# Kernel optimization log

Measured on AMD Instinct MI355X. Metric: run time of the kernel, lower is better.

Reference implementation:

```python
import jax, jax.numpy as jnp
import numpy as np

B, N, D = 8, 2048, 128

def setup_inputs() -> dict:
    key = jax.random.key(0)
    k1, k2, k3 = jax.random.split(key, 3)
    embeddings = jax.random.normal(k1, (B, N, D), dtype=jnp.float32)
    cost_matrix = jax.random.uniform(k2, (B, N, N), dtype=jnp.float32)
    W = jax.random.normal(k3, (D, 2 * D), dtype=jnp.float32) * (1.0 / np.sqrt(2 * D))
    b = jnp.zeros((D,), dtype=jnp.float32)
    return {"embeddings": embeddings, "cost_matrix": cost_matrix, "W": W, "b": b}

def reference(embeddings, cost_matrix, W, b):
    # degree[b,j] = number of nonzero entries in row j of cost_matrix
    degree = (cost_matrix != 0).astype(embeddings.dtype).sum(axis=-1)  # [B,N]
    # sum_neighbors[b,j,d] = sum_i embeddings[b,i,d] * cost_matrix[b,i,j]
    # (algebraic rewrite of the O(B*N*N*D) broadcast-multiply-reduce)
    sum_neighbors = jnp.einsum('bij,bid->bjd', cost_matrix, embeddings)
    sum_neighbors = sum_neighbors / degree[..., None]
    concatenated = jnp.concatenate([embeddings, sum_neighbors], axis=-1)  # [B,N,2D]
    return jax.nn.relu(jnp.einsum('bnf,df->bnd', concatenated, W) + b)
```

## Files before the change

kernel.cpp:

```cpp
#include <hip/hip_runtime.h>
#include <stdint.h>

#define B_ 8
#define N_ 2048
#define D_ 128
#define NT_ 32
#define KT_ 8
#define TILE_BYTES 16384
#define PS_ ((size_t)B_ * N_ * D_)

typedef unsigned short u16;
typedef unsigned int u32;
using f32x4 = __attribute__((ext_vector_type(4))) float;
using bf16x8 = __attribute__((ext_vector_type(8))) short;
using u16x8 = __attribute__((ext_vector_type(8))) u16;

__device__ inline u16 f2bf(float x) {
  u32 u = __float_as_uint(x);
  return (u16)((u + 0x7FFFu + ((u >> 16) & 1u)) >> 16);
}
__device__ inline float bf2f(u16 h) { return __uint_as_float((u32)h << 16); }

__device__ inline void glds16(const void* g, void* l) {
  __builtin_amdgcn_global_load_lds((const __attribute__((address_space(1))) void*)g,
                                   (__attribute__((address_space(3))) void*)l, 16, 0, 0);
}

__global__ __launch_bounds__(256) void prep_kernel(const float* __restrict__ E,
                                                   const float* __restrict__ W,
                                                   u16* __restrict__ ETsw,
                                                   u16* __restrict__ Wfrag) {
  const int blk = blockIdx.x;
  const int t = threadIdx.x;
  if (blk == 256) {
#pragma unroll
    for (int i = 0; i < 16; ++i) {
      const int idx = i * 256 + t;
      const int lane = idx & 63;
      const int kf = (idx >> 6) & 7;
      const int fn = (idx >> 9) & 1;
      const int wv = idx >> 10;
      const int d = wv * 32 + fn * 16 + (lane & 15);
      const int kb = kf * 32 + (lane >> 4) * 8;
      u16x8 pk;
#pragma unroll
      for (int e = 0; e < 8; ++e) pk[e] = f2bf(W[d * 256 + kb + e]);
      *(u16x8*)(Wfrag + (size_t)idx * 8) = pk;
    }
    return;
  }
  __shared__ float Els[64][132];
  const int b = blk >> 5;
  const int g = blk & 31;
  const float* Eb = E + ((size_t)b * N_ + g * 64) * D_;
#pragma unroll
  for (int s = 0; s < 8; ++s) {
    const int f4 = t + 256 * s;
    const int r = f4 >> 5;
    const int c4 = f4 & 31;
    f32x4 v = *(const f32x4*)(Eb + (size_t)r * D_ + c4 * 4);
#pragma unroll
    for (int e = 0; e < 4; ++e) Els[r][c4 * 4 + e] = v[e];
  }
  __syncthreads();
  u16* img = ETsw + ((size_t)b * NT_ + g) * (TILE_BYTES / 2);
  const int d = t >> 1;
  const int swz = (d ^ (d >> 3)) & 7;
#pragma unroll
  for (int gg = 0; gg < 4; ++gg) {
    const int grp = (t & 1) * 4 + gg;
    u16x8 pk;
#pragma unroll
    for (int e = 0; e < 8; ++e) pk[e] = f2bf(Els[grp * 8 + e][d]);
    *(u16x8*)(img + d * 64 + ((grp ^ swz) << 3)) = pk;
  }
}

__global__ __launch_bounds__(256) void gemm_kernel(const float* __restrict__ C,
                                                   const u16* __restrict__ ETsw,
                                                   u16* __restrict__ Sp,
                                                   int* __restrict__ zeros) {
  __shared__ __align__(16) u16 Asw[2][64 * 64];
  __shared__ __align__(16) u16 Bsw[2][128 * 64];
  const int phys = blockIdx.x;
  const int orig = (phys & 7) * 128 + (phys >> 3);
  const int b = orig >> 7;
  const int ks = (orig >> 5) & 3;
  const int jt = orig & 31;
  const int j0 = jt * 64;
  const int t = threadIdx.x;
  const int lane = t & 63;
  const int wave = t >> 6;
  const int wm = wave >> 1, wn = wave & 1;
  const int lm = lane & 15, lh = lane >> 4;
  const int aRow = t >> 4, aCol = t & 15;

  const float* Cb = C + (size_t)b * N_ * N_;
  const char* Eimg = (const char*)(ETsw + (size_t)b * NT_ * (TILE_BYTES / 2));
  int* zb = zeros + b * N_;
  const int g0 = ks * KT_;

  f32x4 acc[2][4];
#pragma unroll
  for (int i = 0; i < 2; ++i)
#pragma unroll
    for (int j = 0; j < 4; ++j) acc[i][j] = (f32x4)0.0f;
  f32x4 av[2][4];

#define ISSUE_B(gi, buf)                                                          \
  {                                                                               \
    _Pragma("unroll") for (int s = 0; s < 4; ++s) {                               \
      const int chunk = s * 4 + wave;                                             \
      glds16(Eimg + (size_t)(gi)*TILE_BYTES + chunk * 1024 + lane * 16,           \
             (char*)&Bsw[buf][0] + chunk * 1024);                                 \
    }                                                                             \
  }
#define LOAD_A(gi, slot)                                                          \
  {                                                                               \
    _Pragma("unroll") for (int s = 0; s < 4; ++s) av[slot][s] =                   \
        *(const f32x4*)(Cb + (size_t)((gi)*64 + aRow + 16 * s) * N_ + j0 + aCol * 4); \
  }
#define WRITE_A(gi, buf, slot)                                                    \
  {                                                                               \
    _Pragma("unroll") for (int s = 0; s < 4; ++s) {                               \
      const int i = aRow + 16 * s;                                                \
      f32x4 v = av[slot][s];                                                      \
      int zc = (v[0] == 0.0f) + (v[1] == 0.0f) + (v[2] == 0.0f) + (v[3] == 0.0f);\
      if (__any(zc)) {                         \
        if (zc) atomicAdd(&zb[(gi)*64 + i], zc);                                  \
      }                                                                           \
      _Pragma("unroll") for (int e = 0; e < 4; ++e) {                             \
        const int jl = aCol * 4 + e;                                              \
        const int sz = (jl ^ (jl >> 3)) & 7;                                      \
        Asw[buf][jl * 64 + (i ^ (sz << 3))] = f2bf(v[e]);                         \
      }                                                                           \
    }                                                                             \
  }
#define MFMA_PHASE(buf)                                                           \
  {                                                                               \
    bf16x8 af[2][2], bfr[4][2];                                                   \
    _Pragma("unroll") for (int fm = 0; fm < 2; ++fm) {                            \
      const int jl = wm * 32 + fm * 16 + lm;                                      \
      const int sz = (jl ^ (jl >> 3)) & 7;                                        \
      _Pragma("unroll") for (int kf = 0; kf < 2; ++kf) {                          \
        const int K8 = kf * 32 + lh * 8;                                          \
        af[fm][kf] = *(const bf16x8*)&Asw[buf][jl * 64 + (K8 ^ (sz << 3))];       \
      }                                                                           \
    }                                                                             \
    _Pragma("unroll") for (int fn = 0; fn < 4; ++fn) {                            \
      const int nl = wn * 64 + fn * 16 + lm;                                      \
      const int sz = (nl ^ (nl >> 3)) & 7;                                        \
      _Pragma("unroll") for (int kf = 0; kf < 2; ++kf) {                          \
        const int K8 = kf * 32 + lh * 8;                                          \
        bfr[fn][kf] = *(const bf16x8*)&Bsw[buf][nl * 64 + (K8 ^ (sz << 3))];      \
      }                                                                           \
    }                                                                             \
    _Pragma("unroll") for (int kf = 0; kf < 2; ++kf)                              \
        _Pragma("unroll") for (int fm = 0; fm < 2; ++fm)                          \
        _Pragma("unroll") for (int fn = 0; fn < 4; ++fn) acc[fm][fn] =            \
        __builtin_amdgcn_mfma_f32_16x16x32_bf16(af[fm][kf], bfr[fn][kf],          \
                                                acc[fm][fn], 0, 0, 0);            \
  }
#define STEP(kt, DOLOAD, VMSTR)                                                   \
  ISSUE_B(g0 + (kt) + 1, ((kt) + 1) & 1);                                         \
  __builtin_amdgcn_sched_barrier(0);                                              \
  MFMA_PHASE((kt) & 1);                                                           \
  __builtin_amdgcn_sched_barrier(0);                                              \
  WRITE_A(g0 + (kt) + 1, ((kt) + 1) & 1, (kt) & 1);                               \
  __builtin_amdgcn_sched_barrier(0);                                              \
  if (DOLOAD) LOAD_A(g0 + (kt) + 3, (kt) & 1);                                    \
  __builtin_amdgcn_sched_barrier(0);                                              \
  asm volatile("s_waitcnt " VMSTR ::: "memory");                                  \
  asm volatile("s_waitcnt lgkmcnt(0)" ::: "memory");                              \
  __builtin_amdgcn_sched_barrier(0);                                              \
  __builtin_amdgcn_s_barrier();                                                   \
  __builtin_amdgcn_sched_barrier(0);

  ISSUE_B(g0, 0);
  LOAD_A(g0, 0);
  WRITE_A(g0, 0, 0);
  LOAD_A(g0 + 1, 0);
  LOAD_A(g0 + 2, 1);
  asm volatile("s_waitcnt lgkmcnt(0)" ::: "memory");
  __builtin_amdgcn_sched_barrier(0);
  __builtin_amdgcn_s_barrier();
  __builtin_amdgcn_sched_barrier(0);

  STEP(0, 1, "vmcnt(4)")
  STEP(1, 1, "vmcnt(4)")
  STEP(2, 1, "vmcnt(4)")
  STEP(3, 1, "vmcnt(4)")
  STEP(4, 1, "vmcnt(4)")
  STEP(5, 0, "vmcnt(0)")
  STEP(6, 0, "vmcnt(0)")
  MFMA_PHASE(1)

  u16* Sb = Sp + (size_t)ks * PS_ + ((size_t)b * N_ + j0) * D_;
#pragma unroll
  for (int fm = 0; fm < 2; ++fm)
#pragma unroll
    for (int fn = 0; fn < 4; ++fn)
#pragma unroll
      for (int r = 0; r < 4; ++r) {
        const int row = wm * 32 + fm * 16 + lh * 4 + r;
        const int col = wn * 64 + fn * 16 + lm;
        Sb[(size_t)row * D_ + col] = f2bf(acc[fm][fn][r]);
      }
#undef ISSUE_B
#undef LOAD_A
#undef WRITE_A
#undef MFMA_PHASE
#undef STEP
}

__global__ __launch_bounds__(256) void out_kernel(const float* __restrict__ E,
                                                  const u16* __restrict__ Sp,
                                                  const int* __restrict__ zeros,
                                                  const u16* __restrict__ Wfrag,
                                                  const float* __restrict__ bias,
                                                  float* __restrict__ out) {
  __shared__ __align__(16) u16 Als[32 * 256];
  const int r0 = blockIdx.x * 32;
  const int t = threadIdx.x;
  const int lane = t & 63;
  const int wave = t >> 6;
  const int lm = lane & 15, lh = lane >> 4;

  bf16x8 wf[2][8];
#pragma unroll
  for (int fn = 0; fn < 2; ++fn)
#pragma unroll
    for (int kf = 0; kf < 8; ++kf)
      wf[fn][kf] = *(const bf16x8*)(Wfrag +
          (((size_t)(wave * 2 + fn) * 8 + kf) * 64 + lane) * 8);

  const int r = t >> 3, gq = t & 7;
  const int swzr = (r ^ (r >> 3)) & 7;
  const float idg = 1.0f / (2048.0f - (float)zeros[r0 + r]);
  const float* Er = E + (size_t)(r0 + r) * D_;
#pragma unroll
  for (int h = 0; h < 2; ++h) {
    const int k8 = gq + 8 * h;
    f32x4 v0 = *(const f32x4*)(Er + k8 * 8);
    f32x4 v1 = *(const f32x4*)(Er + k8 * 8 + 4);
    u16x8 pk;
#pragma unroll
    for (int e = 0; e < 4; ++e) { pk[e] = f2bf(v0[e]); pk[4 + e] = f2bf(v1[e]); }
    *(u16x8*)&Als[r * 256 + ((k8 ^ swzr) << 3)] = pk;
  }
  const size_t off = (size_t)(r0 + r) * D_;
#pragma unroll
  for (int h = 0; h < 2; ++h) {
    const int kq = gq + 8 * h;
    u16x8 p0 = *(const u16x8*)(Sp + 0 * PS_ + off + kq * 8);
    u16x8 p1 = *(const u16x8*)(Sp + 1 * PS_ + off + kq * 8);
    u16x8 p2 = *(const u16x8*)(Sp + 2 * PS_ + off + kq * 8);
    u16x8 p3 = *(const u16x8*)(Sp + 3 * PS_ + off + kq * 8);
    u16x8 pk;
#pragma unroll
    for (int e = 0; e < 8; ++e) {
      float sum = (bf2f(p0[e]) + bf2f(p1[e])) + (bf2f(p2[e]) + bf2f(p3[e]));
      pk[e] = f2bf(sum * idg);
    }
    *(u16x8*)&Als[r * 256 + (((16 + kq) ^ swzr) << 3)] = pk;
  }
  __syncthreads();

  f32x4 acc[2][2];
#pragma unroll
  for (int i = 0; i < 2; ++i)
#pragma unroll
    for (int j = 0; j < 2; ++j) acc[i][j] = (f32x4)0.0f;
  const int dbase = wave * 32;
#pragma unroll
  for (int kf = 0; kf < 8; ++kf) {
    bf16x8 af[2];
#pragma unroll
    for (int fm = 0; fm < 2; ++fm) {
      const int rr = fm * 16 + lm;
      const int sz = (rr ^ (rr >> 3)) & 7;
      af[fm] = *(const bf16x8*)&Als[rr * 256 + (((kf * 4 + lh) ^ sz) << 3)];
    }
#pragma unroll
    for (int fm = 0; fm < 2; ++fm)
#pragma unroll
      for (int fn = 0; fn < 2; ++fn)
        acc[fm][fn] = __builtin_amdgcn_mfma_f32_16x16x32_bf16(af[fm], wf[fn][kf],
                                                              acc[fm][fn], 0, 0, 0);
  }
  float bb[2] = {bias[dbase + lm], bias[dbase + 16 + lm]};
#pragma unroll
  for (int fm = 0; fm < 2; ++fm)
#pragma unroll
    for (int fn = 0; fn < 2; ++fn)
#pragma unroll
      for (int rr = 0; rr < 4; ++rr) {
        const int row = r0 + fm * 16 + lh * 4 + rr;
        const int d = dbase + fn * 16 + lm;
        float x = acc[fm][fn][rr] + bb[fn];
        out[(size_t)row * D_ + d] = x > 0.0f ? x : 0.0f;
      }
}

extern "C" void kernel_launch(void* const* d_in, const int* in_sizes, int n_in,
                              void* d_out, int out_size, void* d_ws, size_t ws_size,
                              hipStream_t stream) {
  (void)in_sizes; (void)n_in; (void)out_size; (void)ws_size;
  const float* E = (const float*)d_in[0];
  const float* C = (const float*)d_in[1];
  const float* W = (const float*)d_in[2];
  const float* bias = (const float*)d_in[3];
  float* out = (float*)d_out;

  char* ws = (char*)d_ws;
  int* zeros = (int*)ws;
  u16* ETsw = (u16*)(ws + 65536);
  u16* Wfrag = (u16*)(ws + 65536 + 4194304);
  u16* Sp = (u16*)(ws + 65536 + 4194304 + 65536);

  hipMemsetAsync(zeros, 0, B_ * N_ * sizeof(int), stream);
  hipLaunchKernelGGL(prep_kernel, dim3(257), dim3(256), 0, stream, E, W, ETsw, Wfrag);
  hipLaunchKernelGGL(gemm_kernel, dim3(1024), dim3(256), 0, stream, C, ETsw, Sp, zeros);
  hipLaunchKernelGGL(out_kernel, dim3(512), dim3(256), 0, stream, E, Sp, zeros, Wfrag, bias, out);
}
```

Before: 223.3 us.

## Reassociate neighbor aggregation to multiply embeddings by W first

The prep kernel now computes E·W1 and G = E·W2 with MFMA. The big cost-matrix GEMM then multiplies C^T by G instead of by E, so the final kernel becomes an elementwise combine: EW1 + H·inv_degree + bias, then ReLU. This removes the second dense GEMM from the output stage. In exchange it adds an fp32 EW1 buffer and rounds G to bf16 before the large GEMM, which changes the rounding error. The dominant C GEMM stays the same size.

```diff
diff --git a/kernel.cpp b/kernel.cpp
--- a/kernel.cpp
+++ b/kernel.cpp
@@ -26,59 +26,107 @@
                                    (__attribute__((address_space(3))) void*)l, 16, 0, 0);
 }
 
-__global__ __launch_bounds__(256) void prep_kernel(const float* __restrict__ E,
-                                                   const float* __restrict__ W,
-                                                   u16* __restrict__ ETsw,
-                                                   u16* __restrict__ Wfrag) {
+__global__ __launch_bounds__(256) void prep2_kernel(const float* __restrict__ E,
+                                                    const float* __restrict__ W,
+                                                    u16* __restrict__ Gimg,
+                                                    float* __restrict__ EW1) {
+  __shared__ __align__(16) u16 SH[64 * 128];
   const int blk = blockIdx.x;
+  const int b = blk >> 5;
+  const int it = blk & 31;
+  const int i0 = it * 64;
   const int t = threadIdx.x;
-  if (blk == 256) {
-#pragma unroll
-    for (int i = 0; i < 16; ++i) {
-      const int idx = i * 256 + t;
-      const int lane = idx & 63;
-      const int kf = (idx >> 6) & 7;
-      const int fn = (idx >> 9) & 1;
-      const int wv = idx >> 10;
-      const int d = wv * 32 + fn * 16 + (lane & 15);
-      const int kb = kf * 32 + (lane >> 4) * 8;
-      u16x8 pk;
-#pragma unroll
-      for (int e = 0; e < 8; ++e) pk[e] = f2bf(W[d * 256 + kb + e]);
-      *(u16x8*)(Wfrag + (size_t)idx * 8) = pk;
+  const int lane = t & 63;
+  const int wave = t >> 6;
+  const int lm = lane & 15, lh = lane >> 4;
+
+  const float* Eb = E + ((size_t)b * N_ + i0) * D_;
+#pragma unroll
+  for (int c = 0; c < 4; ++c) {
+    const int chunk = c * 256 + t;
+    const int i = chunk >> 4;
+    const int k8 = chunk & 15;
+    f32x4 v0 = *(const f32x4*)(Eb + i * D_ + k8 * 8);
+    f32x4 v1 = *(const f32x4*)(Eb + i * D_ + k8 * 8 + 4);
+    u16x8 pk;
+#pragma unroll
+    for (int e = 0; e < 4; ++e) { pk[e] = f2bf(v0[e]); pk[4 + e] = f2bf(v1[e]); }
+    *(u16x8*)&SH[i * 128 + ((k8 ^ (i & 7)) << 3)] = pk;
+  }
+  __syncthreads();
+
+  const int dbase = wave * 32;
+  f32x4 acc1[4][2], accG[4][2];
+#pragma unroll
+  for (int fm = 0; fm < 4; ++fm)
+#pragma unroll
+    for (int fn = 0; fn < 2; ++fn) { acc1[fm][fn] = (f32x4)0.0f; accG[fm][fn] = (f32x4)0.0f; }
+#pragma unroll
+  for (int kf = 0; kf < 4; ++kf) {
+    bf16x8 af[4];
+#pragma unroll
+    for (int fm = 0; fm < 4; ++fm) {
+      const int i = fm * 16 + lm;
+      af[fm] = *(const bf16x8*)&SH[i * 128 + (((kf * 4 + lh) ^ (i & 7)) << 3)];
     }
-    return;
-  }
-  __shared__ float Els[64][132];
-  const int b = blk >> 5;
-  const int g = blk & 31;
-  const float* Eb = E + ((size_t)b * N_ + g * 64) * D_;
-#pragma unroll
-  for (int s = 0; s < 8; ++s) {
-    const int f4 = t + 256 * s;
-    const int r = f4 >> 5;
-    const int c4 = f4 & 31;
-    f32x4 v = *(const f32x4*)(Eb + (size_t)r * D_ + c4 * 4);
-#pragma unroll
-    for (int e = 0; e < 4; ++e) Els[r][c4 * 4 + e] = v[e];
-  }
+#pragma unroll
+    for (int fn = 0; fn < 2; ++fn) {
+      const int d = dbase + fn * 16 + lm;
+      const float* wr = W + d * 256 + kf * 32 + lh * 8;
+      f32x4 a0 = *(const f32x4*)(wr);
+      f32x4 a1 = *(const f32x4*)(wr + 4);
+      f32x4 b0 = *(const f32x4*)(wr + 128);
+      f32x4 b1 = *(const f32x4*)(wr + 132);
+      u16x8 w1, w2;
+#pragma unroll
+      for (int e = 0; e < 4; ++e) {
+        w1[e] = f2bf(a0[e]); w1[4 + e] = f2bf(a1[e]);
+        w2[e] = f2bf(b0[e]); w2[4 + e] = f2bf(b1[e]);
+      }
+      bf16x8 w1f = *(bf16x8*)&w1;
+      bf16x8 w2f = *(bf16x8*)&w2;
+#pragma unroll
+      for (int fm = 0; fm < 4; ++fm) {
+        acc1[fm][fn] = __builtin_amdgcn_mfma_f32_16x16x32_bf16(af[fm], w1f, acc1[fm][fn], 0, 0, 0);
+        accG[fm][fn] = __builtin_amdgcn_mfma_f32_16x16x32_bf16(af[fm], w2f, accG[fm][fn], 0, 0, 0);
+      }
+    }
+  }
+  float* EWb = EW1 + ((size_t)b * N_ + i0) * D_;
+#pragma unroll
+  for (int fm = 0; fm < 4; ++fm)
+#pragma unroll
+    for (int fn = 0; fn < 2; ++fn)
+#pragma unroll
+      for (int rr = 0; rr < 4; ++rr)
+        EWb[(fm * 16 + lh * 4 + rr) * D_ + dbase + fn * 16 + lm] = acc1[fm][fn][rr];
+
   __syncthreads();
-  u16* img = ETsw + ((size_t)b * NT_ + g) * (TILE_BYTES / 2);
+#pragma unroll
+  for (int fm = 0; fm < 4; ++fm)
+#pragma unroll
+    for (int fn = 0; fn < 2; ++fn)
+#pragma unroll
+      for (int rr = 0; rr < 4; ++rr) {
+        const int d = dbase + fn * 16 + lm;
+        const int il = fm * 16 + lh * 4 + rr;
+        SH[d * 64 + ((((il >> 3) ^ (d & 7)) << 3) | (il & 7))] = f2bf(accG[fm][fn][rr]);
+      }
+  __syncthreads();
+  u16* img = Gimg + ((size_t)b * NT_ + it) * (TILE_BYTES / 2);
   const int d = t >> 1;
   const int swz = (d ^ (d >> 3)) & 7;
 #pragma unroll
   for (int gg = 0; gg < 4; ++gg) {
     const int grp = (t & 1) * 4 + gg;
-    u16x8 pk;
-#pragma unroll
-    for (int e = 0; e < 8; ++e) pk[e] = f2bf(Els[grp * 8 + e][d]);
+    u16x8 pk = *(const u16x8*)&SH[d * 64 + ((grp ^ (d & 7)) << 3)];
     *(u16x8*)(img + d * 64 + ((grp ^ swz) << 3)) = pk;
   }
 }
 
 __global__ __launch_bounds__(256) void gemm_kernel(const float* __restrict__ C,
-                                                   const u16* __restrict__ ETsw,
-                                                   u16* __restrict__ Sp,
+                                                   const u16* __restrict__ Gimg,
+                                                   u16* __restrict__ Hp,
                                                    int* __restrict__ zeros) {
   __shared__ __align__(16) u16 Asw[2][64 * 64];
   __shared__ __align__(16) u16 Bsw[2][128 * 64];
@@ -96,7 +144,7 @@
   const int aRow = t >> 4, aCol = t & 15;
 
   const float* Cb = C + (size_t)b * N_ * N_;
-  const char* Eimg = (const char*)(ETsw + (size_t)b * NT_ * (TILE_BYTES / 2));
+  const char* Bimg = (const char*)(Gimg + (size_t)b * NT_ * (TILE_BYTES / 2));
   int* zb = zeros + b * N_;
   const int g0 = ks * KT_;
 
@@ -111,7 +159,7 @@
   {                                                                               \
     _Pragma("unroll") for (int s = 0; s < 4; ++s) {                               \
       const int chunk = s * 4 + wave;                                             \
-      glds16(Eimg + (size_t)(gi)*TILE_BYTES + chunk * 1024 + lane * 16,           \
+      glds16(Bimg + (size_t)(gi)*TILE_BYTES + chunk * 1024 + lane * 16,           \
              (char*)&Bsw[buf][0] + chunk * 1024);                                 \
     }                                                                             \
   }
@@ -195,7 +243,7 @@
   STEP(6, 0, "vmcnt(0)")
   MFMA_PHASE(1)
 
-  u16* Sb = Sp + (size_t)ks * PS_ + ((size_t)b * N_ + j0) * D_;
+  u16* Hb = Hp + (size_t)ks * PS_ + ((size_t)b * N_ + j0) * D_;
 #pragma unroll
   for (int fm = 0; fm < 2; ++fm)
 #pragma unroll
@@ -204,7 +252,7 @@
       for (int r = 0; r < 4; ++r) {
         const int row = wm * 32 + fm * 16 + lh * 4 + r;
         const int col = wn * 64 + fn * 16 + lm;
-        Sb[(size_t)row * D_ + col] = f2bf(acc[fm][fn][r]);
+        Hb[(size_t)row * D_ + col] = f2bf(acc[fm][fn][r]);
       }
 #undef ISSUE_B
 #undef LOAD_A
@@ -213,93 +261,36 @@
 #undef STEP
 }
 
-__global__ __launch_bounds__(256) void out_kernel(const float* __restrict__ E,
-                                                  const u16* __restrict__ Sp,
-                                                  const int* __restrict__ zeros,
-                                                  const u16* __restrict__ Wfrag,
-                                                  const float* __restrict__ bias,
-                                                  float* __restrict__ out) {
-  __shared__ __align__(16) u16 Als[32 * 256];
-  const int r0 = blockIdx.x * 32;
-  const int t = threadIdx.x;
-  const int lane = t & 63;
-  const int wave = t >> 6;
-  const int lm = lane & 15, lh = lane >> 4;
-
-  bf16x8 wf[2][8];
-#pragma unroll
-  for (int fn = 0; fn < 2; ++fn)
-#pragma unroll
-    for (int kf = 0; kf < 8; ++kf)
-      wf[fn][kf] = *(const bf16x8*)(Wfrag +
-          (((size_t)(wave * 2 + fn) * 8 + kf) * 64 + lane) * 8);
-
-  const int r = t >> 3, gq = t & 7;
-  const int swzr = (r ^ (r >> 3)) & 7;
-  const float idg = 1.0f / (2048.0f - (float)zeros[r0 + r]);
-  const float* Er = E + (size_t)(r0 + r) * D_;
-#pragma unroll
-  for (int h = 0; h < 2; ++h) {
-    const int k8 = gq + 8 * h;
-    f32x4 v0 = *(const f32x4*)(Er + k8 * 8);
-    f32x4 v1 = *(const f32x4*)(Er + k8 * 8 + 4);
-    u16x8 pk;
-#pragma unroll
-    for (int e = 0; e < 4; ++e) { pk[e] = f2bf(v0[e]); pk[4 + e] = f2bf(v1[e]); }
-    *(u16x8*)&Als[r * 256 + ((k8 ^ swzr) << 3)] = pk;
-  }
-  const size_t off = (size_t)(r0 + r) * D_;
-#pragma unroll
-  for (int h = 0; h < 2; ++h) {
-    const int kq = gq + 8 * h;
-    u16x8 p0 = *(const u16x8*)(Sp + 0 * PS_ + off + kq * 8);
-    u16x8 p1 = *(const u16x8*)(Sp + 1 * PS_ + off + kq * 8);
-    u16x8 p2 = *(const u16x8*)(Sp + 2 * PS_ + off + kq * 8);
-    u16x8 p3 = *(const u16x8*)(Sp + 3 * PS_ + off + kq * 8);
-    u16x8 pk;
-#pragma unroll
-    for (int e = 0; e < 8; ++e) {
-      float sum = (bf2f(p0[e]) + bf2f(p1[e])) + (bf2f(p2[e]) + bf2f(p3[e]));
-      pk[e] = f2bf(sum * idg);
-    }
-    *(u16x8*)&Als[r * 256 + (((16 + kq) ^ swzr) << 3)] = pk;
-  }
-  __syncthreads();
-
-  f32x4 acc[2][2];
-#pragma unroll
-  for (int i = 0; i < 2; ++i)
-#pragma unroll
-    for (int j = 0; j < 2; ++j) acc[i][j] = (f32x4)0.0f;
-  const int dbase = wave * 32;
-#pragma unroll
-  for (int kf = 0; kf < 8; ++kf) {
-    bf16x8 af[2];
-#pragma unroll
-    for (int fm = 0; fm < 2; ++fm) {
-      const int rr = fm * 16 + lm;
-      const int sz = (rr ^ (rr >> 3)) & 7;
-      af[fm] = *(const bf16x8*)&Als[rr * 256 + (((kf * 4 + lh) ^ sz) << 3)];
-    }
-#pragma unroll
-    for (int fm = 0; fm < 2; ++fm)
-#pragma unroll
-      for (int fn = 0; fn < 2; ++fn)
-        acc[fm][fn] = __builtin_amdgcn_mfma_f32_16x16x32_bf16(af[fm], wf[fn][kf],
-                                                              acc[fm][fn], 0, 0, 0);
-  }
-  float bb[2] = {bias[dbase + lm], bias[dbase + 16 + lm]};
-#pragma unroll
-  for (int fm = 0; fm < 2; ++fm)
-#pragma unroll
-    for (int fn = 0; fn < 2; ++fn)
-#pragma unroll
-      for (int rr = 0; rr < 4; ++rr) {
-        const int row = r0 + fm * 16 + lh * 4 + rr;
-        const int d = dbase + fn * 16 + lm;
-        float x = acc[fm][fn][rr] + bb[fn];
-        out[(size_t)row * D_ + d] = x > 0.0f ? x : 0.0f;
-      }
+__global__ __launch_bounds__(256) void outlite_kernel(const float* __restrict__ EW1,
+                                                      const u16* __restrict__ Hp,
+                                                      const int* __restrict__ zeros,
+                                                      const float* __restrict__ bias,
+                                                      float* __restrict__ out) {
+  const int idx = blockIdx.x * 256 + threadIdx.x;
+  const int row = idx >> 4;
+  const int d8 = idx & 15;
+  const float idg = 1.0f / (2048.0f - (float)zeros[row]);
+  const size_t off = (size_t)row * D_ + d8 * 8;
+  f32x4 e0 = *(const f32x4*)(EW1 + off);
+  f32x4 e1 = *(const f32x4*)(EW1 + off + 4);
+  u16x8 h0 = *(const u16x8*)(Hp + 0 * PS_ + off);
+  u16x8 h1 = *(const u16x8*)(Hp + 1 * PS_ + off);
+  u16x8 h2 = *(const u16x8*)(Hp + 2 * PS_ + off);
+  u16x8 h3 = *(const u16x8*)(Hp + 3 * PS_ + off);
+  f32x4 b0 = *(const f32x4*)(bias + d8 * 8);
+  f32x4 b1 = *(const f32x4*)(bias + d8 * 8 + 4);
+  f32x4 r0, r1;
+#pragma unroll
+  for (int e = 0; e < 4; ++e) {
+    float s0 = (bf2f(h0[e]) + bf2f(h1[e])) + (bf2f(h2[e]) + bf2f(h3[e]));
+    float s1 = (bf2f(h0[4 + e]) + bf2f(h1[4 + e])) + (bf2f(h2[4 + e]) + bf2f(h3[4 + e]));
+    float x0 = e0[e] + s0 * idg + b0[e];
+    float x1 = e1[e] + s1 * idg + b1[e];
+    r0[e] = x0 > 0.0f ? x0 : 0.0f;
+    r1[e] = x1 > 0.0f ? x1 : 0.0f;
+  }
+  *(f32x4*)(out + off) = r0;
+  *(f32x4*)(out + off + 4) = r1;
 }
 
 extern "C" void kernel_launch(void* const* d_in, const int* in_sizes, int n_in,
@@ -314,12 +305,12 @@
 
   char* ws = (char*)d_ws;
   int* zeros = (int*)ws;
-  u16* ETsw = (u16*)(ws + 65536);
-  u16* Wfrag = (u16*)(ws + 65536 + 4194304);
-  u16* Sp = (u16*)(ws + 65536 + 4194304 + 65536);
+  u16* Gimg = (u16*)(ws + 65536);
+  float* EW1 = (float*)(ws + 65536 + 4194304);
+  u16* Hp = (u16*)(ws + 65536 + 4194304 + 8388608);
 
   hipMemsetAsync(zeros, 0, B_ * N_ * sizeof(int), stream);
-  hipLaunchKernelGGL(prep_kernel, dim3(257), dim3(256), 0, stream, E, W, ETsw, Wfrag);
-  hipLaunchKernelGGL(gemm_kernel, dim3(1024), dim3(256), 0, stream, C, ETsw, Sp, zeros);
-  hipLaunchKernelGGL(out_kernel, dim3(512), dim3(256), 0, stream, E, Sp, zeros, Wfrag, bias, out);
-}
+  hipLaunchKernelGGL(prep2_kernel, dim3(256), dim3(256), 0, stream, E, W, Gimg, EW1);
+  hipLaunchKernelGGL(gemm_kernel, dim3(1024), dim3(256), 0, stream, C, Gimg, Hp, zeros);
+  hipLaunchKernelGGL(outlite_kernel, dim3(1024), dim3(256), 0, stream, EW1, Hp, zeros, bias, out);
+}
```

After: 226.0 us. Within noise of the previous version (+1.2%).
